# Kernel optimization log

Hardware: AMD Instinct MI355X
Metric: run time of the kernel (lower is better)

## Reference

```python
import jax, jax.numpy as jnp
from jax import lax
import numpy as np

L = 21                      # total_labels (incl. background class 0)
VARIANCES = (0.1, 0.1, 0.2, 0.2)
NMS_THRESHOLD = 0.5
MAX_TOTAL_SIZE = 200        # also max_output_size_per_class
SCORE_THRESHOLD = 0.5


def setup_inputs() -> dict:
    key = jax.random.key(0)
    k1, k2, k3, k4 = jax.random.split(key, 4)
    B, N = 1, 2048
    # valid normalized rois: y1<y2, x1<x2, inside [0,1]
    yx = jax.random.uniform(k1, (B, N, 2)) * 0.8
    hw = jax.random.uniform(k2, (B, N, 2)) * 0.19 + 0.01
    roi_bboxes = jnp.concatenate([yx, yx + hw], axis=-1)
    pred_deltas = jax.random.normal(k3, (B, N, L * 4)) * 0.2
    pred_label_probs = jax.random.uniform(k4, (B, N, L))
    return {"roi_bboxes": roi_bboxes, "pred_deltas": pred_deltas,
            "pred_label_probs": pred_label_probs}


def _decode(rois, deltas):
    # rois/deltas: (..., 4), boxes [y1,x1,y2,x2], deltas [dy,dx,dh,dw]
    h = rois[..., 2] - rois[..., 0]
    w = rois[..., 3] - rois[..., 1]
    cy = rois[..., 0] + 0.5 * h
    cx = rois[..., 1] + 0.5 * w
    nh = jnp.exp(deltas[..., 2]) * h
    nw = jnp.exp(deltas[..., 3]) * w
    ncy = deltas[..., 0] * h + cy
    ncx = deltas[..., 1] * w + cx
    return jnp.stack([ncy - 0.5 * nh, ncx - 0.5 * nw,
                      ncy + 0.5 * nh, ncx + 0.5 * nw], axis=-1)


def _iou_matrix(b):  # b: (N,4) -> (N,N)
    y1, x1, y2, x2 = b[:, 0], b[:, 1], b[:, 2], b[:, 3]
    area = (y2 - y1) * (x2 - x1)
    ih = jnp.clip(jnp.minimum(y2[:, None], y2[None, :]) - jnp.maximum(y1[:, None], y1[None, :]), 0.0)
    iw = jnp.clip(jnp.minimum(x2[:, None], x2[None, :]) - jnp.maximum(x1[:, None], x1[None, :]), 0.0)
    inter = ih * iw
    return inter / (area[:, None] + area[None, :] - inter + 1e-9)


def _nms_sorted(boxes, scores):
    # greedy per-class NMS; returns boxes/scores sorted by score desc + keep mask
    order = jnp.argsort(-scores)
    b = boxes[order]
    s = scores[order]
    iou = _iou_matrix(lax.stop_gradient(b))  # NMS decisions are non-differentiable
    n = b.shape[0]
    idx = jnp.arange(n)

    def body(i, keep):
        sup = keep[i] & (iou[i] > NMS_THRESHOLD) & (idx > i)
        return keep & jnp.logical_not(sup)

    keep = lax.fori_loop(0, n, body, jnp.ones((n,), bool))
    keep = keep & (jnp.cumsum(keep) <= MAX_TOTAL_SIZE)  # max_output_size_per_class
    return b, s, keep


def reference(roi_bboxes, pred_deltas, pred_label_probs):
    B, N, _ = roi_bboxes.shape  # B == 1 (module's slicing logic assumes it)
    deltas = pred_deltas.reshape(B, N, L, 4) * jnp.asarray(VARIANCES, pred_deltas.dtype)
    rois = jnp.broadcast_to(roi_bboxes[:, :, None, :], (B, N, L, 4))
    boxes = _decode(rois, deltas)  # (B,N,L,4)

    # zero out all class scores for rois whose argmax is background (class 0)
    am = jnp.argmax(pred_label_probs, axis=-1)
    scores = jnp.where((am != 0)[..., None], pred_label_probs, 0.0)

    boxes_c = jnp.transpose(boxes[0], (1, 0, 2))  # (L,N,4)
    scores_c = scores[0].T                         # (L,N)
    b_s, s_s, keep = jax.vmap(_nms_sorted)(boxes_c, scores_c)

    cls = jnp.broadcast_to(jnp.arange(L, dtype=s_s.dtype)[:, None], (L, N))
    flat_b = b_s.reshape(-1, 4)
    flat_s = s_s.reshape(-1)
    flat_c = cls.reshape(-1)

    def select(kmask):
        sc = jnp.where(kmask.reshape(-1), flat_s, -1.0)
        top_sc, top_idx = lax.top_k(sc, MAX_TOTAL_SIZE)
        return top_sc, jnp.clip(flat_b[top_idx], 0.0, 1.0), flat_c[top_idx]

    # thresholded combined NMS result (padded with zeros, like TF CNMS)
    sc_t, b_t, l_t = select(keep & (s_s > SCORE_THRESHOLD))
    valid_t = sc_t > SCORE_THRESHOLD
    out_b = jnp.where(valid_t[:, None], b_t, 0.0)
    out_s = jnp.where(valid_t, sc_t, 0.0)
    out_l = jnp.where(valid_t, l_t, 0.0)

    # fallback: no detections above threshold -> best unthresholded detection
    sc_u, b_u, l_u = select(keep)
    best = sc_u[0]
    have = best >= 0.001
    slot0 = jnp.arange(MAX_TOTAL_SIZE) == 0
    fb_b = jnp.where((slot0 & have)[:, None], b_u[0], 0.0)
    fb_s = jnp.where(slot0 & have, best, 0.0)
    fb_l = jnp.where(slot0 & have, l_u[0], 0.0)

    use_fb = jnp.sum(valid_t) == 0
    fin_b = jnp.where(use_fb, fb_b, out_b)[None]  # (1, MAX_TOTAL_SIZE, 4)
    fin_s = jnp.where(use_fb, fb_s, out_s)[None]  # (1, MAX_TOTAL_SIZE)
    fin_l = jnp.where(use_fb, fb_l, out_l)[None]  # (1, MAX_TOTAL_SIZE)
    return fin_b, fin_l, fin_s
```

## Files before the change

### kernel.cpp

```cpp
#include <hip/hip_runtime.h>
#include <stdint.h>

#define NN 2048
#define LL 21
#define CAP 200
#define TOT (LL * CAP)
#define TMAX 320
#define NCH (TMAX / 64)
#define NBK 1024
#define ARRCAP 1200

typedef unsigned long long u64;
typedef unsigned int u32;

__device__ __forceinline__ u64 shfl_u64(u64 v, int lane) {
    int lo = (int)(u32)(v & 0xFFFFFFFFull);
    int hi = (int)(u32)(v >> 32);
    lo = __shfl(lo, lane);
    hi = __shfl(hi, lane);
    return ((u64)(u32)hi << 32) | (u32)lo;
}

__device__ __forceinline__ u64 shfl_xor_u64(u64 v, int mask) {
    int lo = (int)(u32)(v & 0xFFFFFFFFull);
    int hi = (int)(u32)(v >> 32);
    lo = __shfl_xor(lo, mask);
    hi = __shfl_xor(hi, mask);
    return ((u64)(u32)hi << 32) | (u32)lo;
}

__device__ __forceinline__ float4 clip01(float4 b) {
    b.x = fminf(fmaxf(b.x, 0.0f), 1.0f);
    b.y = fminf(fmaxf(b.y, 0.0f), 1.0f);
    b.z = fminf(fmaxf(b.z, 0.0f), 1.0f);
    b.w = fminf(fmaxf(b.w, 0.0f), 1.0f);
    return b;
}

__device__ __forceinline__ float4 decode_box(const float4 roi, const float4 dd) {
#pragma clang fp contract(off)
    float h  = roi.z - roi.x;
    float w  = roi.w - roi.y;
    float cy = roi.x + 0.5f * h;
    float cx = roi.y + 0.5f * w;
    float d0 = dd.x * 0.1f;
    float d1 = dd.y * 0.1f;
    float d2 = dd.z * 0.2f;
    float d3 = dd.w * 0.2f;
    float nh = (float)exp((double)d2) * h;
    float nw = (float)exp((double)d3) * w;
    float ncy = d0 * h + cy;
    float ncx = d1 * w + cx;
    return make_float4(ncy - 0.5f * nh, ncx - 0.5f * nw, ncy + 0.5f * nh, ncx + 0.5f * nw);
}

__device__ __forceinline__ float area_of(const float4 b) {
#pragma clang fp contract(off)
    return (b.z - b.x) * (b.w - b.y);
}

__device__ __forceinline__ bool iou_gt(const float4 a, const float4 b) {
#pragma clang fp contract(off)
    float areaA = (a.z - a.x) * (a.w - a.y);
    float areaB = (b.z - b.x) * (b.w - b.y);
    float ih = fminf(a.z, b.z) - fmaxf(a.x, b.x);
    ih = fmaxf(ih, 0.0f);
    float iw = fminf(a.w, b.w) - fmaxf(a.y, b.y);
    iw = fmaxf(iw, 0.0f);
    float inter = ih * iw;
    float denom = ((areaA + areaB) - inter) + 1e-9f;
    return (inter / denom) > 0.5f;
}

__device__ __forceinline__ bool iou_gt_pre(const float4 a, const float4 b,
                                           float areaA, float areaB) {
#pragma clang fp contract(off)
    float ih = fminf(a.z, b.z) - fmaxf(a.x, b.x);
    ih = fmaxf(ih, 0.0f);
    float iw = fminf(a.w, b.w) - fmaxf(a.y, b.y);
    iw = fmaxf(iw, 0.0f);
    float inter = ih * iw;
    float denom = ((areaA + areaB) - inter) + 1e-9f;
    return (inter / denom) > 0.5f;
}

__device__ __forceinline__ int rb_of(u64 key) {
    u32 sb = (u32)(key >> 32);
    int rb = 1023 - (int)((sb - 0x3F000000u) >> 13);
    return min(max(rb, 0), 1023);
}

__device__ __forceinline__ u64 lowmask(int n) {
    return (n >= 64) ? ~0ull : ((1ull << n) - 1ull);
}

template <int NTHR>
__device__ __forceinline__ void desc_scan(int* histR, int* dstart, int* cursor,
                                          int* wtot, int t) {
    const int PB = NBK / NTHR;
    const int NW = NTHR / 64;
    const int lane = t & 63, w = t >> 6;
    int c[PB], local = 0;
    for (int k = 0; k < PB; ++k) { c[k] = histR[PB * t + k]; local += c[k]; }
    int incl = local;
    for (int d = 1; d < 64; d <<= 1) {
        int v = __shfl_up(incl, d);
        if (lane >= d) incl += v;
    }
    if (lane == 63) wtot[w] = incl;
    __syncthreads();
    int woff = 0;
    for (int i = 0; i < w && i < NW; ++i) woff += wtot[i];
    int run = woff + incl - local;
    for (int k = 0; k < PB; ++k) {
        dstart[PB * t + k] = run;
        cursor[PB * t + k] = run;
        run += c[k];
    }
    __syncthreads();
}

__global__ __launch_bounds__(256) void score_kernel(
    const float* __restrict__ probs,
    u32* __restrict__ scoreT)
{
    __shared__ float tile[256 * LL];
    const int a0 = blockIdx.x * 256;
    const int t = threadIdx.x;
    const float4* src = (const float4*)probs + blockIdx.x * 1344;
    float4* dst = (float4*)tile;
    for (int i = t; i < 1344; i += 256) dst[i] = src[i];
    __syncthreads();
    const float* row = tile + t * LL;
    float best = row[0];
    int bi = 0;
    for (int j = 1; j < LL; ++j) {
        float v = row[j];
        if (v > best) { best = v; bi = j; }
    }
    for (int c = 0; c < LL; ++c)
        scoreT[c * NN + a0 + t] = (bi != 0) ? __float_as_uint(row[c]) : 0u;
}

#define SMEM_B 64384
#define A1OFF 17408
#define A2OFF 34816
#define A3OFF 47104
#define A4OFF 63104

__global__ __launch_bounds__(1024, 1) void per_class_kernel(
    const u32* __restrict__ scoreT,
    const float* __restrict__ roi,
    const float* __restrict__ deltas,
    u64* __restrict__ cand_key,
    float4* __restrict__ cand_box,
    u64* __restrict__ fb_key,
    float4* __restrict__ fb_box)
{
    const int cls = blockIdx.x;
    const int t = threadIdx.x;
    const int lane = t & 63;

    __shared__ char sm[SMEM_B];
    __shared__ int sCnt, sK;
    __shared__ u64 sGmax;
    __shared__ u64 keepm[NCH];
    __shared__ int wtot[16];

    u64* skey  = (u64*)sm;
    u64* skey3 = (u64*)sm;
    u64* skey2 = (u64*)(sm + A1OFF);
    int* histR  = (int*)(sm + A2OFF);
    int* cursor = (int*)(sm + A2OFF + 4096);
    int* dstart = (int*)(sm + A2OFF + 8192);
    float4* cbox = (float4*)(sm + A3OFF);
    u64* R  = (u64*)(sm + A3OFF + 5120);
    u64* Tm = (u64*)(sm + A3OFF + 7680);
    float4* kept = (float4*)(sm + A3OFF + 12800);
    float* area = (float*)(sm + A4OFF);

    if (t == 0) { sCnt = 0; sK = 0; sGmax = 0ull; }
    if (t < CAP) cand_key[cls * CAP + t] = 0ull;
    histR[t] = 0;
    __syncthreads();

    uint2 s2 = ((const uint2*)(scoreT + cls * NN))[t];
    u32 sv[2] = { s2.x, s2.y };
    u64 lq[2];
    int ln = 0;
    u64 lmax = 0ull;
    for (int k = 0; k < 2; ++k) {
        u32 a = 2 * t + k;
        u64 key = ((u64)sv[k] << 32) | (u32)(~a);
        if (key > lmax) lmax = key;
        if (sv[k] > 0x3F000000u) lq[ln++] = key;
    }
    for (int d = 1; d < 64; d <<= 1) {
        u64 o = shfl_xor_u64(lmax, d);
        if (o > lmax) lmax = o;
    }
    if (lane == 0) atomicMax(&sGmax, lmax);
    int incl = ln;
    for (int d = 1; d < 64; d <<= 1) {
        int v = __shfl_up(incl, d);
        if (lane >= d) incl += v;
    }
    int wsum = __shfl(incl, 63);
    int wbase = 0;
    if (lane == 63) wbase = atomicAdd(&sCnt, wsum);
    wbase = __shfl(wbase, 63);
    int off = wbase + incl - ln;
    for (int j = 0; j < ln; ++j) {
        skey[off + j] = lq[j];
        atomicAdd(&histR[rb_of(lq[j])], 1);
    }
    __syncthreads();
    const int M = sCnt;
    const int TT = min(M, TMAX);

    if (t == 0) {
        u64 g = sGmax;
        u32 a0 = ~(u32)(g & 0xFFFFFFFFull);
        float4 rb = *(const float4*)(roi + a0 * 4);
        float4 dd = *(const float4*)(deltas + a0 * (LL * 4) + cls * 4);
        fb_box[cls] = decode_box(rb, dd);
        fb_key[cls] = (g & 0xFFFFFFFF00000000ull) | (u32)(~(u32)(cls * NN));
    }

    desc_scan<1024>(histR, dstart, cursor, wtot, t);

    for (int i = t; i < M; i += 1024) {
        u64 k = skey[i];
        int pos = atomicAdd(&cursor[rb_of(k)], 1);
        skey2[pos] = k;
    }
    __syncthreads();

    for (int p = t; p < M; p += 1024) {
        u64 k = skey2[p];
        int rb = rb_of(k);
        int s = dstart[rb], e = s + histR[rb];
        int rnk = s;
        for (int q = s; q < e; ++q) rnk += (skey2[q] > k) ? 1 : 0;
        skey3[rnk] = k;
        if (rnk < TT) {
            u32 a = ~(u32)(k & 0xFFFFFFFFull);
            float4 rbx = *(const float4*)(roi + a * 4);
            float4 dd = *(const float4*)(deltas + a * (LL * 4) + cls * 4);
            float4 bx = decode_box(rbx, dd);
            cbox[rnk] = bx;
            area[rnk] = area_of(bx);
        }
    }
    __syncthreads();

    const int NCHe = (TT + 63) / 64;
    const int NJ = NCHe * (NCHe + 1) / 2;

    for (int task = t; task < NJ * 64; task += 1024) {
        const int jobid = task >> 6, j = task & 63;
        int cj = 0, acc = 0;
        while (acc + cj + 1 <= jobid) { acc += cj + 1; ++cj; }
        const int ci = jobid - acc;
        const int gj = cj * 64 + j;
        const int nbj = min(64, TT - cj * 64);
        if (ci == cj) {
            u64 row = 0ull;
            if (j < nbj) {
                float4 bj = cbox[gj];
                float aj = area[gj];
                for (int r2 = j + 1; r2 < nbj; ++r2)
                    if (iou_gt_pre(bj, cbox[cj * 64 + r2], aj, area[cj * 64 + r2]))
                        row |= (1ull << r2);
            }
            R[cj * 64 + j] = row;
        } else {
            u64 wd = 0ull;
            if (j < nbj) {
                float4 bj = cbox[gj];
                float aj = area[gj];
                const float4* cb = cbox + ci * 64;
                const float* ca = area + ci * 64;
                for (int i = 0; i < 64; ++i)
                    if (iou_gt_pre(cb[i], bj, ca[i], aj)) wd |= (1ull << i);
            }
            Tm[(cj * (cj - 1) / 2 + ci) * 64 + j] = wd;
        }
    }
    __syncthreads();

    if (t < 64) {
        int K = 0;
        for (int cj = 0; cj < NCHe; ++cj) {
            if (K >= CAP) break;
            const int nb = min(64, TT - cj * 64);
            u64 row = R[cj * 64 + t];
            bool ext = (t >= nb);
            for (int ci = 0; ci < cj; ++ci)
                if (Tm[(cj * (cj - 1) / 2 + ci) * 64 + t] & keepm[ci]) ext = true;
            u64 rem = __ballot(ext);
            const u64 nz = __ballot(row != 0ull) & ~rem;
            u64 m = nz;
            while (m) {
                int i = __ffsll(m) - 1;
                u64 ri = shfl_u64(row, i);
                rem |= ri;
                u64 gt = (i == 63) ? 0ull : ~lowmask(i + 1);
                m = nz & ~rem & gt;
            }
            u64 keep = ~rem & lowmask(nb);
            if (t == 0) keepm[cj] = keep;
            if (t < nb && ((keep >> t) & 1ull)) {
                int krank = K + __popcll(keep & lowmask(t));
                if (krank < CAP) {
                    kept[krank] = cbox[cj * 64 + t];
                    int slot = cls * CAP + krank;
                    cand_key[slot] = (skey3[cj * 64 + t] & 0xFFFFFFFF00000000ull) |
                                     (u32)(~(u32)slot);
                    cand_box[slot] = cbox[cj * 64 + t];
                }
            }
            K += __popcll(keep);
        }
        if (t == 0) sK = K;
    }
    __syncthreads();

    int K = sK;
    if (K < CAP && M > TT) {
        u64* sup = (u64*)(sm + A1OFF);
        unsigned char* extq = (unsigned char*)(sm + A1OFF + 8192);
        const int g = t >> 6, r = t & 63;
        for (int base = TT; base < M; base += 64) {
            K = sK;
            if (K >= CAP) break;
            const int nb = min(64, M - base);
            if (t < nb) {
                u32 a = ~(u32)(skey3[base + t] & 0xFFFFFFFFull);
                float4 rbx = *(const float4*)(roi + a * 4);
                float4 dd = *(const float4*)(deltas + a * (LL * 4) + cls * 4);
                cbox[t] = decode_box(rbx, dd);
            }
            __syncthreads();
            u64 bits = 0ull;
            if (r < nb) {
                float4 br = cbox[r];
                int lo = max(r + 1, g * 4), hi = min(nb, (g + 1) * 4);
                for (int r2 = lo; r2 < hi; ++r2)
                    if (iou_gt(br, cbox[r2])) bits |= (1ull << r2);
            }
            sup[g * 64 + r] = bits;
            bool f = false;
            if (r < nb) {
                float4 bm = cbox[r];
                int per = (K + 15) >> 4;
                int e0 = g * per, e1 = min(K, e0 + per);
                for (int e = e0; e < e1; ++e)
                    if (iou_gt(kept[e], bm)) { f = true; break; }
            }
            extq[g * 64 + r] = f ? 1 : 0;
            __syncthreads();
            if (t < 64) {
                u64 row = 0ull;
                int extv = 0;
                for (int j = 0; j < 16; ++j) { row |= sup[j * 64 + t]; extv |= extq[j * 64 + t]; }
                bool ext = (t < nb) ? (extv != 0) : true;
                u64 rem = __ballot(ext);
                const u64 nz = __ballot(row != 0ull) & ~rem;
                u64 m = nz;
                while (m) {
                    int i = __ffsll(m) - 1;
                    u64 ri = shfl_u64(row, i);
                    rem |= ri;
                    u64 gt = (i == 63) ? 0ull : ~lowmask(i + 1);
                    m = nz & ~rem & gt;
                }
                u64 keep = ~rem & lowmask(nb);
                if (t < nb && ((keep >> t) & 1ull)) {
                    int krank = K + __popcll(keep & lowmask(t));
                    if (krank < CAP) {
                        kept[krank] = cbox[t];
                        int slot = cls * CAP + krank;
                        cand_key[slot] = (skey3[base + t] & 0xFFFFFFFF00000000ull) |
                                         (u32)(~(u32)slot);
                        cand_box[slot] = cbox[t];
                    }
                }
                if (t == 0) sK = K + __popcll(keep);
            }
            __syncthreads();
        }
    }
}

__global__ __launch_bounds__(512) void topk_kernel(
    const u64* __restrict__ cand_key,
    const float4* __restrict__ cand_box,
    const u64* __restrict__ fb_key,
    const float4* __restrict__ fb_box,
    float* __restrict__ out)
{
    const int t = threadIdx.x;
    __shared__ u64 keys[TOT];
    __shared__ int histR[NBK], cursor[NBK], dstart[NBK];
    __shared__ u64 arr[ARRCAP];
    __shared__ u64 outk[CAP];
    __shared__ int wtot[8];
    __shared__ int sRbstar;

    for (int i = t; i < NBK; i += 512) histR[i] = 0;
    if (t < CAP) outk[t] = 0ull;
    if (t == 0) sRbstar = NBK - 1;
    __syncthreads();

    const ulong2* ck2 = (const ulong2*)cand_key;
    for (int i = t; i < TOT / 2; i += 512) {
        ulong2 k2 = ck2[i];
        keys[2 * i]     = k2.x;
        keys[2 * i + 1] = k2.y;
        if (k2.x != 0ull) atomicAdd(&histR[rb_of(k2.x)], 1);
        if (k2.y != 0ull) atomicAdd(&histR[rb_of(k2.y)], 1);
    }
    __syncthreads();
    desc_scan<512>(histR, dstart, cursor, wtot, t);
    for (int k = 0; k < 2; ++k) {
        int rb = 2 * t + k;
        if (dstart[rb] < CAP && dstart[rb] + histR[rb] >= CAP) sRbstar = rb;
    }
    __syncthreads();
    const int rbstar = sRbstar;

    for (int i = t; i < TOT; i += 512) {
        u64 k = keys[i];
        if (k != 0ull) {
            int rb = rb_of(k);
            if (rb <= rbstar) {
                int pos = atomicAdd(&cursor[rb], 1);
                if (pos < ARRCAP) arr[pos] = k;
            }
        }
    }
    __syncthreads();

    const int E = min(dstart[rbstar] + histR[rbstar], ARRCAP);
    for (int p = t; p < E; p += 512) {
        u64 k = arr[p];
        int rb = rb_of(k);
        int s = dstart[rb], e = min(s + histR[rb], ARRCAP);
        int rnk = s;
        for (int q = s; q < e; ++q) rnk += (arr[q] > k) ? 1 : 0;
        if (rnk < CAP) outk[rnk] = k;
    }
    __syncthreads();

    for (int o = t; o < CAP; o += 512) {
        u64 key = outk[o];
        float4 b = make_float4(0.0f, 0.0f, 0.0f, 0.0f);
        float lab = 0.0f, sc = 0.0f;
        if (key != 0ull) {
            u32 slot = ~(u32)(key & 0xFFFFFFFFull);
            sc = __uint_as_float((u32)(key >> 32));
            lab = (float)(slot / CAP);
            b = clip01(cand_box[slot]);
        }
        out[o * 4 + 0] = b.x;
        out[o * 4 + 1] = b.y;
        out[o * 4 + 2] = b.z;
        out[o * 4 + 3] = b.w;
        out[4 * CAP + o] = lab;
        out[5 * CAP + o] = sc;
    }
    __syncthreads();

    if (t == 0 && outk[0] == 0ull) {
        u64 best = 0ull;
        int bc = 0;
        for (int c = 0; c < LL; ++c) {
            u64 k = fb_key[c];
            if (k > best) { best = k; bc = c; }
        }
        float bs = __uint_as_float((u32)(best >> 32));
        if (bs >= 0.001f) {
            float4 bb = clip01(fb_box[bc]);
            out[0] = bb.x; out[1] = bb.y; out[2] = bb.z; out[3] = bb.w;
            out[4 * CAP] = (float)bc;
            out[5 * CAP] = bs;
        }
    }
}

extern "C" void kernel_launch(void* const* d_in, const int* in_sizes, int n_in,
                              void* d_out, int out_size, void* d_ws, size_t ws_size,
                              hipStream_t stream) {
    const float* roi    = (const float*)d_in[0];
    const float* deltas = (const float*)d_in[1];
    const float* probs  = (const float*)d_in[2];
    float* out = (float*)d_out;

    char* ws = (char*)d_ws;
    u32*    scoreT   = (u32*)ws;
    u64*    cand_key = (u64*)(ws + 172032);
    float4* cand_box = (float4*)(ws + 205632);
    u64*    fb_key   = (u64*)(ws + 272832);
    float4* fb_box   = (float4*)(ws + 273008);

    score_kernel<<<NN / 256, 256, 0, stream>>>(probs, scoreT);
    per_class_kernel<<<LL, 1024, 0, stream>>>(scoreT, roi, deltas,
                                              cand_key, cand_box, fb_key, fb_box);
    topk_kernel<<<1, 512, 0, stream>>>(cand_key, cand_box, fb_key, fb_box, out);
}
```

Before: 87.63 us.

## Fuse score transpose into per-class kernel with grid barrier; build top-k histogram globally

Drops the separate score kernel. The first 16 per-class blocks now do the argmax and transpose, and all 21 blocks meet at a global atomic-counter barrier before reading the scores. The per-class kernel also accumulates the radix-bucket histogram of candidate keys into global memory with atomics. The top-k kernel then skips its key-staging and histogram pass and streams keys directly. This removes one launch and a pass over 4200 keys, but adds a memset, a spin barrier that assumes all 21 blocks are co-resident, and global atomic contention.

Result: slower. 95.81 us (+9.3%).

```diff
diff --git a/kernel.cpp b/kernel.cpp
--- a/kernel.cpp
+++ b/kernel.cpp
@@ -120,28 +120,6 @@
     __syncthreads();
 }
 
-__global__ __launch_bounds__(256) void score_kernel(
-    const float* __restrict__ probs,
-    u32* __restrict__ scoreT)
-{
-    __shared__ float tile[256 * LL];
-    const int a0 = blockIdx.x * 256;
-    const int t = threadIdx.x;
-    const float4* src = (const float4*)probs + blockIdx.x * 1344;
-    float4* dst = (float4*)tile;
-    for (int i = t; i < 1344; i += 256) dst[i] = src[i];
-    __syncthreads();
-    const float* row = tile + t * LL;
-    float best = row[0];
-    int bi = 0;
-    for (int j = 1; j < LL; ++j) {
-        float v = row[j];
-        if (v > best) { best = v; bi = j; }
-    }
-    for (int c = 0; c < LL; ++c)
-        scoreT[c * NN + a0 + t] = (bi != 0) ? __float_as_uint(row[c]) : 0u;
-}
-
 #define SMEM_B 64384
 #define A1OFF 17408
 #define A2OFF 34816
@@ -149,13 +127,16 @@
 #define A4OFF 63104
 
 __global__ __launch_bounds__(1024, 1) void per_class_kernel(
-    const u32* __restrict__ scoreT,
+    const float* __restrict__ probs,
     const float* __restrict__ roi,
     const float* __restrict__ deltas,
+    u32* __restrict__ scoreT,
     u64* __restrict__ cand_key,
     float4* __restrict__ cand_box,
     u64* __restrict__ fb_key,
-    float4* __restrict__ fb_box)
+    float4* __restrict__ fb_box,
+    u32* __restrict__ ctr,
+    u32* __restrict__ ghist)
 {
     const int cls = blockIdx.x;
     const int t = threadIdx.x;
@@ -182,10 +163,41 @@
     if (t == 0) { sCnt = 0; sK = 0; sGmax = 0ull; }
     if (t < CAP) cand_key[cls * CAP + t] = 0ull;
     histR[t] = 0;
-    __syncthreads();
-
-    uint2 s2 = ((const uint2*)(scoreT + cls * NN))[t];
-    u32 sv[2] = { s2.x, s2.y };
+
+    if (cls < 16) {
+        float* tile = (float*)sm;
+        const int a0 = cls * 128;
+        const float4* src = (const float4*)(probs + a0 * LL);
+        float4* dst = (float4*)tile;
+        if (t < 672) dst[t] = src[t];
+        __syncthreads();
+        if (t < 128) {
+            const float* row = tile + t * LL;
+            float best = row[0];
+            int bi = 0;
+            for (int j = 1; j < LL; ++j) {
+                float v = row[j];
+                if (v > best) { best = v; bi = j; }
+            }
+            for (int c = 0; c < LL; ++c)
+                scoreT[c * NN + a0 + t] = (bi != 0) ? __float_as_uint(row[c]) : 0u;
+        }
+        __syncthreads();
+    }
+
+    __threadfence();
+    if (t == 0) {
+        __hip_atomic_fetch_add(&ctr[0], 1u, __ATOMIC_ACQ_REL, __HIP_MEMORY_SCOPE_AGENT);
+        while (__hip_atomic_load(&ctr[0], __ATOMIC_ACQUIRE, __HIP_MEMORY_SCOPE_AGENT)
+               < (u32)LL) {}
+    }
+    __syncthreads();
+
+    u32 sv[2];
+    sv[0] = __hip_atomic_load(scoreT + cls * NN + 2 * t,     __ATOMIC_RELAXED,
+                              __HIP_MEMORY_SCOPE_AGENT);
+    sv[1] = __hip_atomic_load(scoreT + cls * NN + 2 * t + 1, __ATOMIC_RELAXED,
+                              __HIP_MEMORY_SCOPE_AGENT);
     u64 lq[2];
     int ln = 0;
     u64 lmax = 0ull;
@@ -315,9 +327,11 @@
                 if (krank < CAP) {
                     kept[krank] = cbox[cj * 64 + t];
                     int slot = cls * CAP + krank;
-                    cand_key[slot] = (skey3[cj * 64 + t] & 0xFFFFFFFF00000000ull) |
-                                     (u32)(~(u32)slot);
+                    u64 key = (skey3[cj * 64 + t] & 0xFFFFFFFF00000000ull) |
+                              (u32)(~(u32)slot);
+                    cand_key[slot] = key;
                     cand_box[slot] = cbox[cj * 64 + t];
+                    atomicAdd(&ghist[rb_of(key)], 1u);
                 }
             }
             K += __popcll(keep);
@@ -381,9 +395,11 @@
                     if (krank < CAP) {
                         kept[krank] = cbox[t];
                         int slot = cls * CAP + krank;
-                        cand_key[slot] = (skey3[base + t] & 0xFFFFFFFF00000000ull) |
-                                         (u32)(~(u32)slot);
+                        u64 key = (skey3[base + t] & 0xFFFFFFFF00000000ull) |
+                                  (u32)(~(u32)slot);
+                        cand_key[slot] = key;
                         cand_box[slot] = cbox[t];
+                        atomicAdd(&ghist[rb_of(key)], 1u);
                     }
                 }
                 if (t == 0) sK = K + __popcll(keep);
@@ -398,30 +414,22 @@
     const float4* __restrict__ cand_box,
     const u64* __restrict__ fb_key,
     const float4* __restrict__ fb_box,
+    const u32* __restrict__ ghist,
     float* __restrict__ out)
 {
     const int t = threadIdx.x;
-    __shared__ u64 keys[TOT];
     __shared__ int histR[NBK], cursor[NBK], dstart[NBK];
     __shared__ u64 arr[ARRCAP];
     __shared__ u64 outk[CAP];
     __shared__ int wtot[8];
     __shared__ int sRbstar;
 
-    for (int i = t; i < NBK; i += 512) histR[i] = 0;
+    histR[2 * t]     = (int)ghist[2 * t];
+    histR[2 * t + 1] = (int)ghist[2 * t + 1];
     if (t < CAP) outk[t] = 0ull;
     if (t == 0) sRbstar = NBK - 1;
     __syncthreads();
 
-    const ulong2* ck2 = (const ulong2*)cand_key;
-    for (int i = t; i < TOT / 2; i += 512) {
-        ulong2 k2 = ck2[i];
-        keys[2 * i]     = k2.x;
-        keys[2 * i + 1] = k2.y;
-        if (k2.x != 0ull) atomicAdd(&histR[rb_of(k2.x)], 1);
-        if (k2.y != 0ull) atomicAdd(&histR[rb_of(k2.y)], 1);
-    }
-    __syncthreads();
     desc_scan<512>(histR, dstart, cursor, wtot, t);
     for (int k = 0; k < 2; ++k) {
         int rb = 2 * t + k;
@@ -430,13 +438,21 @@
     __syncthreads();
     const int rbstar = sRbstar;
 
-    for (int i = t; i < TOT; i += 512) {
-        u64 k = keys[i];
-        if (k != 0ull) {
-            int rb = rb_of(k);
+    const ulong2* ck2 = (const ulong2*)cand_key;
+    for (int i = t; i < TOT / 2; i += 512) {
+        ulong2 k2 = ck2[i];
+        if (k2.x != 0ull) {
+            int rb = rb_of(k2.x);
             if (rb <= rbstar) {
                 int pos = atomicAdd(&cursor[rb], 1);
-                if (pos < ARRCAP) arr[pos] = k;
+                if (pos < ARRCAP) arr[pos] = k2.x;
+            }
+        }
+        if (k2.y != 0ull) {
+            int rb = rb_of(k2.y);
+            if (rb <= rbstar) {
+                int pos = atomicAdd(&cursor[rb], 1);
+                if (pos < ARRCAP) arr[pos] = k2.y;
             }
         }
     }
@@ -503,9 +519,12 @@
     float4* cand_box = (float4*)(ws + 205632);
     u64*    fb_key   = (u64*)(ws + 272832);
     float4* fb_box   = (float4*)(ws + 273008);
-
-    score_kernel<<<NN / 256, 256, 0, stream>>>(probs, scoreT);
-    per_class_kernel<<<LL, 1024, 0, stream>>>(scoreT, roi, deltas,
-                                              cand_key, cand_box, fb_key, fb_box);
-    topk_kernel<<<1, 512, 0, stream>>>(cand_key, cand_box, fb_key, fb_box, out);
-}
+    u32*    ctr      = (u32*)(ws + 273344);
+    u32*    ghist    = (u32*)(ws + 273352);
+
+    (void)hipMemsetAsync(ctr, 0, 8 + NBK * 4, stream);
+    per_class_kernel<<<LL, 1024, 0, stream>>>(probs, roi, deltas, scoreT,
+                                              cand_key, cand_box, fb_key, fb_box,
+                                              ctr, ghist);
+    topk_kernel<<<1, 512, 0, stream>>>(cand_key, cand_box, fb_key, fb_box, ghist, out);
+}
```
